# Performance work log

Hardware: AMD Instinct MI355X
Metric: run time of the kernel (lower is better)

## Reference

```python
import jax, jax.numpy as jnp
import numpy as np

# norse default LIFParameters
DT = 1e-3
TAU_SYN_INV = 200.0
TAU_MEM_INV = 100.0
V_LEAK = 0.0
V_TH = 1.0
V_RESET = 0.0


def heaviside(x):
    return (x > 0).astype(x.dtype)


def setup_inputs() -> dict:
    key = jax.random.key(0)
    ks = jax.random.split(key, 5)
    T, B, I, H, O = 14, 4096, 2048, 1024, 128
    x = (jax.random.uniform(ks[0], (T, B, I), dtype=jnp.float32) < 0.2).astype(jnp.float32)  # spike train
    w_in = jax.random.normal(ks[1], (H, I), dtype=jnp.float32) * (1.0 / np.sqrt(I))
    w_rec = jax.random.normal(ks[2], (H, H), dtype=jnp.float32) * (1.0 / np.sqrt(H))
    out_w = jax.random.normal(ks[3], (O, H), dtype=jnp.float32) * (1.0 / np.sqrt(H))
    out_b = jax.random.normal(ks[4], (O,), dtype=jnp.float32) * 0.01
    return {"x": x, "w_in": w_in, "w_rec": w_rec, "out_w": out_w, "out_b": out_b}


def reference(x, w_in, w_rec, out_w, out_b):
    T, B, _ = x.shape
    H = w_in.shape[0]
    z0 = jnp.zeros((B, H), dtype=x.dtype)
    v0 = jnp.full((B, H), V_LEAK, dtype=x.dtype)
    i0 = jnp.zeros((B, H), dtype=x.dtype)

    def step(carry, x_t):
        z, v, i = carry
        v_dec = v + DT * TAU_MEM_INV * ((V_LEAK - v) + i)   # membrane integration
        i_dec = i - DT * TAU_SYN_INV * i                    # synaptic decay
        z_new = heaviside(v_dec - V_TH)                     # spike
        v_new = (1.0 - z_new) * v_dec + z_new * V_RESET     # reset
        i_new = i_dec + x_t @ w_in.T + z @ w_rec.T          # input + recurrent current
        return (z_new, v_new, i_new), None

    (z_T, _, _), _ = jax.lax.scan(step, (z0, v0, i0), x)
    return z_T @ out_w.T + out_b
```

## Files before the change

### kernel.cpp

```cpp
#include <hip/hip_runtime.h>
#include <hip/hip_cooperative_groups.h>
#include <stdint.h>

namespace cg = cooperative_groups;

#define T_STEPS 14
#define B_DIM   4096
#define I_DIM   2048
#define H_DIM   1024
#define O_DIM   128
#define K_TOT   3072

#define WSCALE_F 33554432.0f

typedef __bf16  bf16x8  __attribute__((ext_vector_type(8)));
typedef float   floatx4 __attribute__((ext_vector_type(4)));
typedef int     int4v   __attribute__((ext_vector_type(4)));
typedef int     int16v  __attribute__((ext_vector_type(16)));

__device__ __forceinline__ uint16_t f2bf_rne(float f) {
    uint32_t u = __float_as_uint(f);
    u += 0x7fffu + ((u >> 16) & 1u);
    return (uint16_t)(u >> 16);
}
__device__ __forceinline__ float bf2f(uint16_t h) {
    return __uint_as_float(((uint32_t)h) << 16);
}

__device__ __forceinline__ void gload_lds16(const void* g, void* l) {
    __builtin_amdgcn_global_load_lds((__attribute__((address_space(1))) void*)g,
                                     (__attribute__((address_space(3))) void*)l, 16, 0, 0);
}


__global__ void split_w_kernel(const float* __restrict__ w_in, const float* __restrict__ w_rec,
                               int8_t* __restrict__ WB) {
    int idx = blockIdx.x * 256 + threadIdx.x;
    int h = idx / K_TOT;
    int k = idx - h * K_TOT;
    float w = (k < I_DIM) ? w_in[(size_t)h * I_DIM + k]
                          : w_rec[(size_t)h * H_DIM + (k - I_DIM)];
    int W  = __float2int_rn(w * WSCALE_F);
    int d0 = (int8_t)(W & 0xFF);
    int r1 = (W - d0) >> 8;
    int d1 = (int8_t)(r1 & 0xFF);
    int d2 = (r1 - d1) >> 8;
    int nt = h >> 5, n32 = h & 31;
    int ktw = k >> 7, k128 = k & 127;
    int kk = k128 >> 5, half = (k128 >> 4) & 1, j = k128 & 15;
    int lane = half * 32 + n32;
    size_t base = (size_t)(nt * 24 + ktw) * 12288 + kk * 1024 + lane * 16 + j;
    WB[base] = (int8_t)d0; WB[base + 4096] = (int8_t)d1; WB[base + 8192] = (int8_t)d2;
}

__global__ void split_ow_kernel(const float* __restrict__ out_w, uint16_t* __restrict__ OW3) {
    int idx = blockIdx.x * 256 + threadIdx.x;
    float w = out_w[idx];
    uint16_t hi = f2bf_rne(w);
    float r1 = w - bf2f(hi);
    uint16_t mid = f2bf_rne(r1);
    float r2 = r1 - bf2f(mid);
    uint16_t lo = f2bf_rne(r2);
    const size_t S = (size_t)O_DIM * H_DIM;
    OW3[idx] = hi; OW3[idx + S] = mid; OW3[idx + 2 * S] = lo;
}

__global__ void cvt_x_kernel(const float* __restrict__ x, int8_t* __restrict__ xb) {
    size_t gid = (size_t)blockIdx.x * 256 + threadIdx.x;
    int g = (int)(gid & 1023);
    size_t chunk = gid >> 10;
    int kt   = (int)(chunk & 15);
    int mIdx = (int)((chunk >> 4) & 31);
    int t    = (int)(chunk >> 9);
    int group = g >> 8, kk = (g >> 6) & 3, lane = g & 63;
    int half = lane >> 5, row32 = lane & 31;
    int b = mIdx * 128 + group * 32 + row32;
    int k = kt * 128 + kk * 32 + half * 16;
    const float4* src = (const float4*)(x + ((size_t)t * B_DIM + b) * I_DIM + k);
    union { int8_t bytes[16]; int4v v; } u;
#pragma unroll
    for (int q = 0; q < 4; ++q) {
        float4 f = src[q];
        u.bytes[q * 4 + 0] = (int8_t)(f.x > 0.5f);
        u.bytes[q * 4 + 1] = (int8_t)(f.y > 0.5f);
        u.bytes[q * 4 + 2] = (int8_t)(f.z > 0.5f);
        u.bytes[q * 4 + 3] = (int8_t)(f.w > 0.5f);
    }
    ((int4v*)xb)[gid] = u.v;
}

__device__ __forceinline__ void lif_iter(const int8_t* __restrict__ aP,
                                         const int8_t* __restrict__ bPn,
                                         const int8_t* cur, int8_t* nxt,
                                         int wave, int lane, bool stage_next,
                                         int16v (&acc)[3]) {
    int4v a0 = *(const int4v*)(aP);
    int4v a1 = *(const int4v*)(aP + 1024);
    int4v a2 = *(const int4v*)(aP + 2048);
    int4v a3 = *(const int4v*)(aP + 3072);
    __builtin_amdgcn_sched_barrier(0);
    if (stage_next) {
        gload_lds16(bPn + (size_t)wave * 1024 + lane * 16,       nxt + wave * 1024);
        gload_lds16(bPn + (size_t)(4 + wave) * 1024 + lane * 16, nxt + (4 + wave) * 1024);
        gload_lds16(bPn + (size_t)(8 + wave) * 1024 + lane * 16, nxt + (8 + wave) * 1024);
        asm volatile("s_waitcnt vmcnt(7)" ::: "memory");
    } else {
        asm volatile("s_waitcnt vmcnt(4)" ::: "memory");
    }
    __builtin_amdgcn_s_barrier();
    __builtin_amdgcn_sched_barrier(0);
#pragma unroll
    for (int kk = 0; kk < 4; ++kk) {
        int4v aF = (kk == 0) ? a0 : (kk == 1) ? a1 : (kk == 2) ? a2 : a3;
#pragma unroll
        for (int s = 0; s < 3; ++s) {
            int4v bF = *(const int4v*)(cur + s * 4096 + kk * 1024 + lane * 16);
            acc[s] = __builtin_amdgcn_mfma_i32_32x32x32_i8(aF, bF, acc[s], 0, 0, 0);
        }
    }
    asm volatile("s_waitcnt lgkmcnt(0)" ::: "memory");
    __builtin_amdgcn_s_barrier();
}

template<int NKT>
__device__ __forceinline__ void run_phase(const int8_t* __restrict__ aChunk0,
                                          const int8_t* __restrict__ bChunk0,
                                          int8_t* sB0, int8_t* sB1,
                                          int wave, int lane, int16v (&acc)[3]) {
    gload_lds16(bChunk0 + (size_t)wave * 1024 + lane * 16,       sB0 + wave * 1024);
    gload_lds16(bChunk0 + (size_t)(4 + wave) * 1024 + lane * 16, sB0 + (4 + wave) * 1024);
    gload_lds16(bChunk0 + (size_t)(8 + wave) * 1024 + lane * 16, sB0 + (8 + wave) * 1024);
    const int8_t* aW = aChunk0 + wave * 4096 + lane * 16;
#pragma unroll 1
    for (int kt = 0; kt + 2 < NKT; kt += 2) {
        lif_iter(aW + (size_t)kt * 16384,       bChunk0 + (size_t)(kt + 1) * 12288, sB0, sB1, wave, lane, true, acc);
        lif_iter(aW + (size_t)(kt + 1) * 16384, bChunk0 + (size_t)(kt + 2) * 12288, sB1, sB0, wave, lane, true, acc);
    }
    lif_iter(aW + (size_t)(NKT - 2) * 16384, bChunk0 + (size_t)(NKT - 1) * 12288, sB0, sB1, wave, lane, true, acc);
    lif_iter(aW + (size_t)(NKT - 1) * 16384, nullptr,                             sB1, sB0, wave, lane, false, acc);
}

__launch_bounds__(256, 4)
__global__ void lif_persist_kernel(const int8_t* __restrict__ Xall,
                                   const int8_t* __restrict__ WB,
                                   int8_t* __restrict__ Z0,
                                   int8_t* __restrict__ Z1,
                                   uint16_t* __restrict__ Zbf) {
    __shared__ int8_t sB0[12288];
    __shared__ int8_t sB1[12288];

    const int tid  = threadIdx.x;
    const int wave = tid >> 6, lane = tid & 63;
    const int lane32 = lane & 31, hl = lane >> 5;

    const int nt = blockIdx.x & 31, mIdx = blockIdx.x >> 5;
    const int mBase = mIdx * 128, nBase = nt * 32;
    const int8_t* wbStrip = WB + (size_t)nt * 24 * 12288;

    float vmem[16], isyn[16];
#pragma unroll
    for (int r = 0; r < 16; ++r) { vmem[r] = 0.0f; isyn[r] = 0.0f; }

    int8_t* zA = Z0;
    int8_t* zB = Z1;

    for (int t = 0; t < T_STEPS; ++t) {
        int16v acc[3] = {};

        const int8_t* Xt = Xall + (size_t)t * ((size_t)B_DIM * I_DIM) + (size_t)mIdx * 16 * 16384;
        run_phase<16>(Xt, wbStrip, sB0, sB1, wave, lane, acc);

        if (t > 0) {
            cg::this_grid().sync();
            run_phase<8>(zA + (size_t)mIdx * 8 * 16384, wbStrip + (size_t)16 * 12288,
                         sB0, sB1, wave, lane, acc);
        }

        int8_t* zchunk = zB + ((size_t)mIdx * 8 + (nt >> 2)) * 16384;
#pragma unroll
        for (int r = 0; r < 16; ++r) {
#pragma clang fp contract(off)
            float cur = (float)acc[2][r] * (1.0f / 512.0f)
                      + (float)acc[1][r] * (1.0f / 131072.0f)
                      + (float)acc[0][r] * (1.0f / 33554432.0f);
            int row = (r & 3) + 8 * (r >> 2) + 4 * hl;
            float v_dec = vmem[r] + 0.1f * ((0.0f - vmem[r]) + isyn[r]);
            float i_dec = isyn[r] - 0.2f * isyn[r];
            bool z = (v_dec > 1.0f);
            vmem[r] = z ? 0.0f : v_dec;
            isyn[r] = i_dec + cur;
            if (t == T_STEPS - 1) {
                int b = mBase + wave * 32 + row;
                int h = nBase + lane32;
                Zbf[(size_t)b * H_DIM + h] = z ? (uint16_t)0x3F80 : (uint16_t)0;
            } else {
                zchunk[wave * 4096 + (nt & 3) * 1024
                       + ((lane32 >> 4) * 32 + row) * 16 + (lane32 & 15)]
                    = z ? (int8_t)1 : (int8_t)0;
            }
        }

        int8_t* tmp = zA; zA = zB; zB = tmp;
    }
}

__launch_bounds__(256, 4)
__global__ void lif_step_kernel(const int8_t* __restrict__ Xt,
                                const int8_t* __restrict__ Zin,
                                const int8_t* __restrict__ WB,
                                float2* __restrict__ VI,
                                int8_t* __restrict__ Zout,
                                uint16_t* __restrict__ Zbf, int t) {
    __shared__ int8_t sA[16384];
    __shared__ int8_t sB[12288];

    const int tid  = threadIdx.x;
    const int wave = tid >> 6, lane = tid & 63;
    const int lane32 = lane & 31, hl = lane >> 5;

    const int nt = blockIdx.x & 31, mIdx = blockIdx.x >> 5;
    const int mBase = mIdx * 128, nBase = nt * 32;

    int16v acc[3] = {};

    const int nIters = (t > 0) ? 24 : 16;

    for (int kt = 0; kt < nIters; ++kt) {
        __syncthreads();
        const int8_t* chunkA = (kt < 16)
            ? Xt  + ((size_t)mIdx * 16 + kt) * 16384
            : Zin + ((size_t)mIdx * 8 + (kt - 16)) * 16384;
#pragma unroll
        for (int j = 0; j < 4; ++j) {
            const int seg = j * 4 + wave;
            gload_lds16(chunkA + seg * 1024 + lane * 16, &sA[seg * 1024]);
        }
        const int8_t* chunkB = WB + (size_t)(nt * 24 + kt) * 12288;
#pragma unroll
        for (int j = 0; j < 3; ++j) {
            const int seg = j * 4 + wave;
            gload_lds16(chunkB + seg * 1024 + lane * 16, &sB[seg * 1024]);
        }
        __syncthreads();
#pragma unroll
        for (int kk = 0; kk < 4; ++kk) {
            int4v aF = *(const int4v*)&sA[wave * 4096 + kk * 1024 + lane * 16];
#pragma unroll
            for (int s = 0; s < 3; ++s) {
                int4v bF = *(const int4v*)&sB[s * 4096 + kk * 1024 + lane * 16];
                acc[s] = __builtin_amdgcn_mfma_i32_32x32x32_i8(aF, bF, acc[s], 0, 0, 0);
            }
        }
    }

    int8_t* zchunk = Zout + ((size_t)mIdx * 8 + (nt >> 2)) * 16384;
#pragma unroll
    for (int r = 0; r < 16; ++r) {
#pragma clang fp contract(off)
        float cur = (float)acc[2][r] * (1.0f / 512.0f)
                  + (float)acc[1][r] * (1.0f / 131072.0f)
                  + (float)acc[0][r] * (1.0f / 33554432.0f);
        int row = (r & 3) + 8 * (r >> 2) + 4 * hl;
        int b = mBase + wave * 32 + row;
        int h = nBase + lane32;
        size_t idx = (size_t)b * H_DIM + h;
        float v, ii;
        if (t == 0) { v = 0.0f; ii = 0.0f; }
        else        { float2 vi = VI[idx]; v = vi.x; ii = vi.y; }
        float v_dec = v + 0.1f * ((0.0f - v) + ii);
        float i_dec = ii - 0.2f * ii;
        bool z = (v_dec > 1.0f);
        float2 vi_new;
        vi_new.x = z ? 0.0f : v_dec;
        vi_new.y = i_dec + cur;
        VI[idx] = vi_new;
        if (t == T_STEPS - 1) {
            Zbf[idx] = z ? (uint16_t)0x3F80 : (uint16_t)0;
        } else {
            zchunk[wave * 4096 + (nt & 3) * 1024
                   + ((lane32 >> 4) * 32 + row) * 16 + (lane32 & 15)]
                = z ? (int8_t)1 : (int8_t)0;
        }
    }
}

__launch_bounds__(256)
__global__ void out_gemm_kernel(const uint16_t* __restrict__ Zfin,
                                const uint16_t* __restrict__ OW3,
                                const float* __restrict__ out_b,
                                float* __restrict__ out) {
    __shared__ uint16_t sA[16 * 32];
    __shared__ uint16_t sB[3][128 * 32];

    const int tid  = threadIdx.x;
    const int wave = tid >> 6, lane = tid & 63;
    const int quad = lane >> 4, col = lane & 15;

    const int mBase = blockIdx.x * 16;

    floatx4 acc[2] = {};

    const int ldRow = lane >> 2;
    const int ldCol = (lane & 3) * 8;

    for (int kt = 0; kt < H_DIM / 32; ++kt) {
        const int kb = kt * 32;
        __syncthreads();
        if (wave == 0) {
            const uint16_t* g = Zfin + (size_t)(mBase + ldRow) * H_DIM + kb + ldCol;
            gload_lds16(g, &sA[0]);
        }
#pragma unroll
        for (int s = 0; s < 3; ++s) {
            const uint16_t* wsrc = OW3 + (size_t)s * O_DIM * H_DIM;
#pragma unroll
            for (int j = 0; j < 2; ++j) {
                const int rseg = j * 4 + wave;
                const uint16_t* g = wsrc + (size_t)(rseg * 16 + ldRow) * H_DIM + kb + ldCol;
                gload_lds16(g, &sB[s][rseg * 16 * 32]);
            }
        }
        __syncthreads();

        bf16x8 aF = *reinterpret_cast<const bf16x8*>(&sA[col * 32 + quad * 8]);
#pragma unroll
        for (int s = 0; s < 3; ++s) {
#pragma unroll
            for (int ni = 0; ni < 2; ++ni) {
                int row = wave * 32 + ni * 16 + col;
                bf16x8 bF = *reinterpret_cast<const bf16x8*>(&sB[s][row * 32 + quad * 8]);
                acc[ni] = __builtin_amdgcn_mfma_f32_16x16x32_bf16(aF, bF, acc[ni], 0, 0, 0);
            }
        }
    }

    {
#pragma clang fp contract(off)
#pragma unroll
        for (int ni = 0; ni < 2; ++ni)
#pragma unroll
            for (int r = 0; r < 4; ++r) {
                int b = mBase + quad * 4 + r;
                int h = wave * 32 + ni * 16 + col;
                out[(size_t)b * O_DIM + h] = acc[ni][r] + out_b[h];
            }
    }
}

extern "C" void kernel_launch(void* const* d_in, const int* in_sizes, int n_in,
                              void* d_out, int out_size, void* d_ws, size_t ws_size,
                              hipStream_t stream) {
    const float* x     = (const float*)d_in[0];
    const float* w_in  = (const float*)d_in[1];
    const float* w_rec = (const float*)d_in[2];
    const float* out_w = (const float*)d_in[3];
    const float* out_b = (const float*)d_in[4];
    float* out = (float*)d_out;

    char* ws = (char*)d_ws;
    size_t off = 0;
    int8_t*   WB   = (int8_t*)(ws + off);   off += (size_t)3 * H_DIM * K_TOT;
    uint16_t* OW3  = (uint16_t*)(ws + off); off += (size_t)3 * O_DIM * H_DIM * 2;
    int8_t*   Xall = (int8_t*)(ws + off);   off += (size_t)T_STEPS * B_DIM * I_DIM;
    uint16_t* Zbf  = (uint16_t*)(ws + off); off += (size_t)B_DIM * H_DIM * 2;
    int8_t*   Z0   = (int8_t*)(ws + off);   off += (size_t)B_DIM * H_DIM;
    int8_t*   Z1   = (int8_t*)(ws + off);   off += (size_t)B_DIM * H_DIM;
    float2*   VI   = (float2*)(ws + off);   off += (size_t)B_DIM * H_DIM * 8;

    split_w_kernel<<<(H_DIM * K_TOT) / 256, 256, 0, stream>>>(w_in, w_rec, WB);
    split_ow_kernel<<<(O_DIM * H_DIM) / 256, 256, 0, stream>>>(out_w, OW3);
    cvt_x_kernel<<<(int)(((size_t)T_STEPS * B_DIM * I_DIM / 16) / 256), 256, 0, stream>>>(x, Xall);

    static int coop_ok = -1;
    if (coop_ok < 0) {
        int dev = 0, v = 0;
        (void)hipGetDevice(&dev);
        if (hipDeviceGetAttribute(&v, hipDeviceAttributeCooperativeLaunch, dev) != hipSuccess) v = 0;
        coop_ok = v;
    }

    bool launched = false;
    if (coop_ok) {
        void* args[] = { (void*)&Xall, (void*)&WB, (void*)&Z0, (void*)&Z1, (void*)&Zbf };
        hipError_t e = hipLaunchCooperativeKernel((const void*)lif_persist_kernel,
                                                  dim3(1024), dim3(256), args, 0, stream);
        if (e == hipSuccess) launched = true;
        else coop_ok = 0;
    }
    if (!launched) {
        int8_t* zbuf[2] = { Z0, Z1 };
        for (int t = 0; t < T_STEPS; ++t) {
            lif_step_kernel<<<dim3(1024), 256, 0, stream>>>(
                Xall + (size_t)t * B_DIM * I_DIM, zbuf[t & 1], WB, VI,
                zbuf[(t + 1) & 1], Zbf, t);
        }
    }

    out_gemm_kernel<<<B_DIM / 16, 256, 0, stream>>>(Zbf, OW3, out_b, out);
}
```

Before: 1.350 ms.

## Replace grid-wide sync with per-row-block spike counters and per-step spike buffers

Each block now waits only on the 32 column blocks of its own batch row-block, using an atomic counter per (row-block, timestep), in place of a full cooperative grid sync. Spike outputs go to a separate buffer per timestep, so there is no write-after-read hazard and no global barrier is needed. Spikes are staged in LDS and written with coalesced 16-byte stores. Block IDs are also remapped, apparently so that related tiles land on different XCDs. The aim is to cut barrier stalls and let row-blocks drift apart in time. The memory ordering rests on relaxed atomics plus a spin-wait with no explicit fences, which risks correctness.

Result: no change. 1.373 ms (+1.8%).

```diff
diff --git a/kernel.cpp b/kernel.cpp
--- a/kernel.cpp
+++ b/kernel.cpp
@@ -1,8 +1,5 @@
 #include <hip/hip_runtime.h>
-#include <hip/hip_cooperative_groups.h>
 #include <stdint.h>
-
-namespace cg = cooperative_groups;
 
 #define T_STEPS 14
 #define B_DIM   4096
@@ -10,6 +7,7 @@
 #define H_DIM   1024
 #define O_DIM   128
 #define K_TOT   3072
+#define ZBYTES  ((size_t)B_DIM * H_DIM)
 
 #define WSCALE_F 33554432.0f
 
@@ -89,6 +87,10 @@
     ((int4v*)xb)[gid] = u.v;
 }
 
+__global__ void zero_cnt_kernel(uint32_t* __restrict__ cnt) {
+    cnt[blockIdx.x * 256 + threadIdx.x] = 0;
+}
+
 __device__ __forceinline__ void lif_iter(const int8_t* __restrict__ aP,
                                          const int8_t* __restrict__ bPn,
                                          const int8_t* cur, int8_t* nxt,
@@ -143,17 +145,22 @@
 __launch_bounds__(256, 4)
 __global__ void lif_persist_kernel(const int8_t* __restrict__ Xall,
                                    const int8_t* __restrict__ WB,
-                                   int8_t* __restrict__ Z0,
-                                   int8_t* __restrict__ Z1,
-                                   uint16_t* __restrict__ Zbf) {
+                                   int8_t* __restrict__ ZS,
+                                   uint16_t* __restrict__ Zbf,
+                                   uint32_t* __restrict__ cnt) {
     __shared__ int8_t sB0[12288];
     __shared__ int8_t sB1[12288];
+    __shared__ int8_t sZ[4096];
 
     const int tid  = threadIdx.x;
     const int wave = tid >> 6, lane = tid & 63;
     const int lane32 = lane & 31, hl = lane >> 5;
 
-    const int nt = blockIdx.x & 31, mIdx = blockIdx.x >> 5;
+    const int bid = blockIdx.x;
+    const int xs = bid & 7, q = bid >> 3;
+    const int mIdx = (xs & 1) * 16 + (q & 15);
+    const int nt   = (xs >> 1) * 8 + (q >> 4);
+
     const int mBase = mIdx * 128, nBase = nt * 32;
     const int8_t* wbStrip = WB + (size_t)nt * 24 * 12288;
 
@@ -161,9 +168,6 @@
 #pragma unroll
     for (int r = 0; r < 16; ++r) { vmem[r] = 0.0f; isyn[r] = 0.0f; }
 
-    int8_t* zA = Z0;
-    int8_t* zB = Z1;
-
     for (int t = 0; t < T_STEPS; ++t) {
         int16v acc[3] = {};
 
@@ -171,12 +175,16 @@
         run_phase<16>(Xt, wbStrip, sB0, sB1, wave, lane, acc);
 
         if (t > 0) {
-            cg::this_grid().sync();
-            run_phase<8>(zA + (size_t)mIdx * 8 * 16384, wbStrip + (size_t)16 * 12288,
-                         sB0, sB1, wave, lane, acc);
-        }
-
-        int8_t* zchunk = zB + ((size_t)mIdx * 8 + (nt >> 2)) * 16384;
+            if (tid == 0) {
+                const uint32_t* f = cnt + ((size_t)mIdx * 13 + (t - 1)) * 32;
+                while (__hip_atomic_load(f, __ATOMIC_RELAXED, __HIP_MEMORY_SCOPE_AGENT) < 32u)
+                    __builtin_amdgcn_s_sleep(2);
+            }
+            __syncthreads();
+            const int8_t* zPrev = ZS + (size_t)(t - 1) * ZBYTES + (size_t)mIdx * 8 * 16384;
+            run_phase<8>(zPrev, wbStrip + (size_t)16 * 12288, sB0, sB1, wave, lane, acc);
+        }
+
 #pragma unroll
         for (int r = 0; r < 16; ++r) {
 #pragma clang fp contract(off)
@@ -194,13 +202,24 @@
                 int h = nBase + lane32;
                 Zbf[(size_t)b * H_DIM + h] = z ? (uint16_t)0x3F80 : (uint16_t)0;
             } else {
-                zchunk[wave * 4096 + (nt & 3) * 1024
-                       + ((lane32 >> 4) * 32 + row) * 16 + (lane32 & 15)]
+                sZ[wave * 1024 + ((lane32 >> 4) * 32 + row) * 16 + (lane32 & 15)]
                     = z ? (int8_t)1 : (int8_t)0;
             }
         }
 
-        int8_t* tmp = zA; zA = zB; zB = tmp;
+        if (t < T_STEPS - 1) {
+            __syncthreads();
+            const unsigned long long* sp = (const unsigned long long*)&sZ[tid * 16];
+            unsigned long long v0 = sp[0], v1 = sp[1];
+            int8_t* dst = ZS + (size_t)t * ZBYTES + ((size_t)mIdx * 8 + (nt >> 2)) * 16384
+                        + (tid >> 6) * 4096 + (nt & 3) * 1024 + (tid & 63) * 16;
+            __hip_atomic_store((unsigned long long*)dst,       v0, __ATOMIC_RELAXED, __HIP_MEMORY_SCOPE_AGENT);
+            __hip_atomic_store((unsigned long long*)(dst + 8), v1, __ATOMIC_RELAXED, __HIP_MEMORY_SCOPE_AGENT);
+            __syncthreads();
+            if (tid == 0)
+                __hip_atomic_fetch_add(&cnt[((size_t)mIdx * 13 + t) * 32], 1u,
+                                       __ATOMIC_RELAXED, __HIP_MEMORY_SCOPE_AGENT);
+        }
     }
 }
 
@@ -363,13 +382,14 @@
     uint16_t* OW3  = (uint16_t*)(ws + off); off += (size_t)3 * O_DIM * H_DIM * 2;
     int8_t*   Xall = (int8_t*)(ws + off);   off += (size_t)T_STEPS * B_DIM * I_DIM;
     uint16_t* Zbf  = (uint16_t*)(ws + off); off += (size_t)B_DIM * H_DIM * 2;
-    int8_t*   Z0   = (int8_t*)(ws + off);   off += (size_t)B_DIM * H_DIM;
-    int8_t*   Z1   = (int8_t*)(ws + off);   off += (size_t)B_DIM * H_DIM;
+    int8_t*   ZS   = (int8_t*)(ws + off);   off += (size_t)13 * ZBYTES;
+    uint32_t* CNT  = (uint32_t*)(ws + off); off += (size_t)32 * 13 * 32 * 4;
     float2*   VI   = (float2*)(ws + off);   off += (size_t)B_DIM * H_DIM * 8;
 
     split_w_kernel<<<(H_DIM * K_TOT) / 256, 256, 0, stream>>>(w_in, w_rec, WB);
     split_ow_kernel<<<(O_DIM * H_DIM) / 256, 256, 0, stream>>>(out_w, OW3);
     cvt_x_kernel<<<(int)(((size_t)T_STEPS * B_DIM * I_DIM / 16) / 256), 256, 0, stream>>>(x, Xall);
+    zero_cnt_kernel<<<(32 * 13 * 32) / 256, 256, 0, stream>>>(CNT);
 
     static int coop_ok = -1;
     if (coop_ok < 0) {
@@ -381,14 +401,14 @@
 
     bool launched = false;
     if (coop_ok) {
-        void* args[] = { (void*)&Xall, (void*)&WB, (void*)&Z0, (void*)&Z1, (void*)&Zbf };
+        void* args[] = { (void*)&Xall, (void*)&WB, (void*)&ZS, (void*)&Zbf, (void*)&CNT };
         hipError_t e = hipLaunchCooperativeKernel((const void*)lif_persist_kernel,
                                                   dim3(1024), dim3(256), args, 0, stream);
         if (e == hipSuccess) launched = true;
         else coop_ok = 0;
     }
     if (!launched) {
-        int8_t* zbuf[2] = { Z0, Z1 };
+        int8_t* zbuf[2] = { ZS, ZS + ZBYTES };
         for (int t = 0; t < T_STEPS; ++t) {
             lif_step_kernel<<<dim3(1024), 256, 0, stream>>>(
                 Xall + (size_t)t * B_DIM * I_DIM, zbuf[t & 1], WB, VI,
```
